# Performance work log

Measured on AMD Instinct MI355X. Metric: run time of the kernel, lower is better.

Reference implementation:

```python
import jax, jax.numpy as jnp
import numpy as np

SL, BS, D, H = 2048, 4, 512, 8
NH = D // H  # per-head dim (nhid)
SCALE = np.float32(1.0 / np.sqrt(NH))


def setup_inputs() -> dict:
    key = jax.random.key(0)
    ks = jax.random.split(key, 8)
    s = np.float32(0.02)
    return {
        "input_tensor": jax.random.normal(ks[0], (SL, BS, D), jnp.float32),
        "keys_vector": jax.random.normal(ks[1], (SL, BS, D), jnp.float32),
        "values_vector": jax.random.normal(ks[2], (SL, BS, D), jnp.float32),
        # learned projections: query/keys/values -> num_heads*nhid, plus output proj
        "Wq": jax.random.normal(ks[3], (D, D), jnp.float32) * s,
        "bq": jnp.zeros((D,), jnp.float32),
        "Wk": jax.random.normal(ks[4], (D, D), jnp.float32) * s,
        "bk": jnp.zeros((D,), jnp.float32),
        "Wv": jax.random.normal(ks[5], (D, D), jnp.float32) * s,
        "bv": jnp.zeros((D,), jnp.float32),
        "Wo": jax.random.normal(ks[6], (D, D), jnp.float32) * s,
        "bo": jnp.zeros((D,), jnp.float32),
    }


def reference(input_tensor, keys_vector, values_vector, Wq, bq, Wk, bk, Wv, bv, Wo, bo):
    # Vectorized equivalent of the per-step Python loop with incremental mask
    # (mask=True): query step i attends to keys 0..i -> causal attention.
    q = (input_tensor @ Wq + bq).reshape(SL, BS, H, NH)   # [q,b,h,n]
    k = (keys_vector @ Wk + bk).reshape(SL, BS, H, NH)    # [s,b,h,n]
    v = (values_vector @ Wv + bv).reshape(SL, BS, H, NH)  # [s,b,h,n]
    scores = jnp.einsum('qbhn,sbhn->qsbh', q, k) * SCALE  # [q,s,b,h]
    causal = jnp.tril(jnp.ones((SL, SL), dtype=bool))     # allow s <= q
    scores = jnp.where(causal[:, :, None, None], scores, jnp.float32(-1e9))
    w = jax.nn.softmax(scores, axis=1)                    # softmax over keys s
    out = jnp.einsum('qsbh,sbhn->qbhn', w, v).reshape(SL, BS, D)
    return out @ Wo + bo                                  # [q,b,D]
```

## Files before the change

kernel.cpp:

```cpp
#include <hip/hip_runtime.h>

typedef __attribute__((ext_vector_type(8))) short short8;
typedef __attribute__((ext_vector_type(4))) short short4v;
typedef __attribute__((ext_vector_type(4))) float f32x4;
typedef __attribute__((ext_vector_type(2))) unsigned int uint2v;

constexpr int SL = 2048, BS = 4, D = 512, H = 8, NH = 64;
constexpr int M_ROWS = SL * BS;
constexpr float SCALE = 0.125f;
constexpr float LOG2E = 1.44269504088896340736f;

__device__ __forceinline__ unsigned short f2bf(float f) {
  union { float f; unsigned u; } v; v.f = f;
  unsigned r = v.u + 0x7FFFu + ((v.u >> 16) & 1u);
  return (unsigned short)(r >> 16);
}

__device__ __forceinline__ unsigned cvt_pk_bf16(float a, float b) {
  unsigned r;
  asm("v_cvt_pk_bf16_f32 %0, %1, %2" : "=v"(r) : "v"(a), "v"(b));
  return r;
}

__device__ __forceinline__ float fast_exp2(float x) {
  float r;
  asm("v_exp_f32 %0, %1" : "=v"(r) : "v"(x));
  return r;
}

__device__ __forceinline__ void gl16(const void* g, void* l) {
  __builtin_amdgcn_global_load_lds(
      (const __attribute__((address_space(1))) unsigned int*)g,
      (__attribute__((address_space(3))) unsigned int*)l, 16, 0, 0);
}

__global__ __launch_bounds__(256) void prep_wt(
    const float* __restrict__ w0, const float* __restrict__ w1,
    const float* __restrict__ w2, const float* __restrict__ w3,
    unsigned short* __restrict__ wtb) {
  __shared__ float tl[64][65];
  const int tid = threadIdx.x;
  const int wi = blockIdx.x >> 6, t6 = blockIdx.x & 63;
  const int k0 = (t6 >> 3) * 64, n0 = (t6 & 7) * 64;
  const float* W = wi == 0 ? w0 : (wi == 1 ? w1 : (wi == 2 ? w2 : w3));
  unsigned short* WT = wtb + (size_t)wi * D * D;

#pragma unroll
  for (int i = 0; i < 4; ++i) {
    int k = (tid >> 4) + i * 16, n4 = (tid & 15) * 4;
    f32x4 v = *reinterpret_cast<const f32x4*>(&W[(size_t)(k0 + k) * D + n0 + n4]);
#pragma unroll
    for (int j = 0; j < 4; ++j) tl[n4 + j][k] = v[j];
  }
  __syncthreads();
#pragma unroll
  for (int i = 0; i < 2; ++i) {
    int n = (tid >> 3) + i * 32, k8 = (tid & 7) * 8;
    union { unsigned u[4]; short8 s; } pk;
#pragma unroll
    for (int j = 0; j < 4; ++j)
      pk.u[j] = cvt_pk_bf16(tl[n][k8 + 2 * j], tl[n][k8 + 2 * j + 1]);
    *reinterpret_cast<short8*>(&WT[(size_t)(n0 + n) * D + k0 + k8]) = pk.s;
  }
}

template <bool A_BF16, int OUT_MODE>
__device__ __forceinline__ void gemm_bt_body(const void* __restrict__ Ap,
                                             const unsigned short* __restrict__ BT,
                                             const float* __restrict__ bias,
                                             void* __restrict__ Outp, float scale,
                                             unsigned short* smem) {
  const int tid = threadIdx.x;
  const int brow = blockIdx.x * 128;
  const int bcol = blockIdx.y * 128;
  const int lane = tid & 63;
  const int wid = tid >> 6;
  const int wr = (wid >> 1) * 64;
  const int wc = (wid & 1) * 64;
  const int r = lane & 15;
  const int g = lane >> 4;

  auto a_buf = [&](int b) { return smem + b * 16384; };
  auto b_buf = [&](int b) { return smem + b * 16384 + 8192; };

  f32x4 acc[4][4];
#pragma unroll
  for (int m = 0; m < 4; ++m)
#pragma unroll
    for (int n = 0; n < 4; ++n) acc[m][n] = f32x4{0.f, 0.f, 0.f, 0.f};

  auto STAGE_B = [&](int kt, int bsel) {
    unsigned short* bl = b_buf(bsel);
#pragma unroll
    for (int j = 0; j < 4; ++j) {
      int c = j * 256 + tid;
      int row = c >> 3, c8 = (c & 7) ^ (row & 7);
      gl16(&BT[(size_t)(bcol + row) * D + kt + c8 * 8], &bl[c * 8]);
    }
  };
  auto STAGE_A_LDS = [&](int kt, int bsel) {
    const unsigned short* A = (const unsigned short*)Ap;
    unsigned short* al = a_buf(bsel);
#pragma unroll
    for (int j = 0; j < 4; ++j) {
      int c = j * 256 + tid;
      int row = c >> 3, c8 = (c & 7) ^ (row & 7);
      gl16(&A[(size_t)(brow + row) * D + kt + c8 * 8], &al[c * 8]);
    }
  };
  auto A_LOAD = [&](int kt, f32x4 (&va)[4][2]) {
    const float* A = (const float*)Ap;
#pragma unroll
    for (int j = 0; j < 4; ++j) {
      int c = j * 256 + tid;
      int row = c >> 3, c8 = (c & 7) ^ (row & 7);
      const float* ap = &A[(size_t)(brow + row) * D + kt + c8 * 8];
      va[j][0] = *reinterpret_cast<const f32x4*>(ap);
      va[j][1] = *reinterpret_cast<const f32x4*>(ap + 4);
    }
  };
  auto A_WRITE = [&](f32x4 (&va)[4][2], int bsel) {
    unsigned short* al = a_buf(bsel);
#pragma unroll
    for (int j = 0; j < 4; ++j) {
      int c = j * 256 + tid;
      union { unsigned u[4]; short8 s; } pk;
      pk.u[0] = cvt_pk_bf16(va[j][0][0], va[j][0][1]);
      pk.u[1] = cvt_pk_bf16(va[j][0][2], va[j][0][3]);
      pk.u[2] = cvt_pk_bf16(va[j][1][0], va[j][1][1]);
      pk.u[3] = cvt_pk_bf16(va[j][1][2], va[j][1][3]);
      *reinterpret_cast<short8*>(&al[c * 8]) = pk.s;
    }
  };
  auto COMPUTE = [&](int bsel) {
    const unsigned short* al = a_buf(bsel);
    const unsigned short* bl = b_buf(bsel);
#pragma unroll
    for (int kk2 = 0; kk2 < 2; ++kk2) {
      short8 af[4], bfr[4];
#pragma unroll
      for (int m = 0; m < 4; ++m)
        af[m] = *reinterpret_cast<const short8*>(
            &al[(wr + m * 16 + r) * 64 + (((kk2 * 4 + g) ^ (r & 7)) * 8)]);
#pragma unroll
      for (int n = 0; n < 4; ++n)
        bfr[n] = *reinterpret_cast<const short8*>(
            &bl[(wc + n * 16 + r) * 64 + (((kk2 * 4 + g) ^ (r & 7)) * 8)]);
      __builtin_amdgcn_s_setprio(1);
#pragma unroll
      for (int m = 0; m < 4; ++m)
#pragma unroll
        for (int n = 0; n < 4; ++n)
          acc[m][n] = __builtin_amdgcn_mfma_f32_16x16x32_bf16(af[m], bfr[n], acc[m][n], 0, 0, 0);
      __builtin_amdgcn_s_setprio(0);
    }
  };

  if (A_BF16) {
    STAGE_A_LDS(0, 0);
    STAGE_B(0, 0);
    asm volatile("s_waitcnt vmcnt(0)" ::: "memory");
  } else {
    f32x4 va[4][2];
    A_LOAD(0, va);
    STAGE_B(0, 0);
    asm volatile("s_waitcnt vmcnt(4)" ::: "memory");
    A_WRITE(va, 0);
    asm volatile("s_waitcnt vmcnt(0) lgkmcnt(0)" ::: "memory");
  }
  __builtin_amdgcn_s_barrier();

#pragma unroll
  for (int t = 0; t < 8; ++t) {
    const int cur = t & 1, nxt = cur ^ 1;
    const int ktn = (t + 1) * 64;
    __builtin_amdgcn_sched_barrier(0);
    f32x4 va[4][2];
    if (t < 7) {
      if (A_BF16) {
        STAGE_A_LDS(ktn, nxt);
        STAGE_B(ktn, nxt);
      } else {
        A_LOAD(ktn, va);
        STAGE_B(ktn, nxt);
      }
    }
    __builtin_amdgcn_sched_barrier(0);
    COMPUTE(cur);
    if (t < 7) {
      if (!A_BF16) {
        asm volatile("s_waitcnt vmcnt(4)" ::: "memory");
        A_WRITE(va, nxt);
      }
      asm volatile("s_waitcnt vmcnt(0) lgkmcnt(0)" ::: "memory");
      __builtin_amdgcn_s_barrier();
    }
  }

  if (OUT_MODE == 2) {
    unsigned short* sc = smem;
    const int wr4 = wr >> 2;
#pragma unroll
    for (int m = 0; m < 4; ++m)
#pragma unroll
      for (int n = 0; n < 4; ++n) {
        int col = wc + n * 16 + r;
        float bv = bias[bcol + col];
        int sl = wr4 + m * 4 + g;
#pragma unroll
        for (int rr = 0; rr < 4; ++rr) {
          int c = (rr * 4 + (sl >> 3)) ^ (col & 7);
          sc[col * 128 + c * 8 + (sl & 7)] = f2bf((acc[m][n][rr] + bv) * scale);
        }
      }
    asm volatile("s_waitcnt lgkmcnt(0)" ::: "memory");
    __builtin_amdgcn_s_barrier();
    unsigned short* VT = (unsigned short*)Outp;
#pragma unroll
    for (int i2 = 0; i2 < 2; ++i2) {
      int q = tid * 2 + i2;
      int col = q >> 2, bb = q & 3;
      int gcol = bcol + col, hh = gcol >> 6, nh = gcol & 63;
      size_t gbase = (((size_t)bb * H + hh) * NH + nh) * SL + (brow >> 2);
#pragma unroll
      for (int j = 0; j < 4; ++j) {
        short8 v = *reinterpret_cast<const short8*>(
            &sc[col * 128 + (((bb * 4 + j) ^ (col & 7)) * 8)]);
        *reinterpret_cast<short8*>(&VT[gbase + j * 8]) = v;
      }
    }
  } else {
#pragma unroll
    for (int m = 0; m < 4; ++m)
#pragma unroll
      for (int n = 0; n < 4; ++n) {
        int gcol = bcol + wc + n * 16 + r;
        float bv = bias[gcol];
#pragma unroll
        for (int rr = 0; rr < 4; ++rr) {
          int grow = brow + wr + m * 16 + g * 4 + rr;
          float val = (acc[m][n][rr] + bv) * scale;
          if (OUT_MODE == 0)
            ((float*)Outp)[(size_t)grow * D + gcol] = val;
          else
            ((unsigned short*)Outp)[(size_t)grow * D + gcol] = f2bf(val);
        }
      }
  }
}

__global__ __launch_bounds__(256, 2) void qkv_gemm(
    const float* __restrict__ x0, const float* __restrict__ x1, const float* __restrict__ x2,
    const unsigned short* __restrict__ wtb,
    const float* __restrict__ b0, const float* __restrict__ b1, const float* __restrict__ b2,
    unsigned short* __restrict__ q_out, unsigned short* __restrict__ k_out,
    unsigned short* __restrict__ vt_out) {
  __shared__ __align__(16) unsigned short smem[2 * 16384];
  int z = blockIdx.z;
  const float* X = z == 0 ? x0 : (z == 1 ? x1 : x2);
  const unsigned short* WT = wtb + (size_t)z * D * D;
  const float* B = z == 0 ? b0 : (z == 1 ? b1 : b2);
  float scale = (z == 0) ? SCALE * LOG2E : 1.0f;
  if (z == 2)
    gemm_bt_body<false, 2>(X, WT, B, vt_out, scale, smem);
  else
    gemm_bt_body<false, 1>(X, WT, B, z == 0 ? q_out : k_out, scale, smem);
}

__global__ __launch_bounds__(256, 2) void gemm_oproj(
    const unsigned short* __restrict__ A, const unsigned short* __restrict__ WT,
    const float* __restrict__ B, float* __restrict__ Outp) {
  __shared__ __align__(16) unsigned short smem[2 * 16384];
  gemm_bt_body<true, 0>(A, WT, B, Outp, 1.0f, smem);
}

__global__ __launch_bounds__(256, 4) void flash_attn(
    const unsigned short* __restrict__ Q, const unsigned short* __restrict__ K,
    const unsigned short* __restrict__ Vt, unsigned short* __restrict__ O) {
  __shared__ __align__(16) unsigned short k_lds[2][64 * 64];
  __shared__ __align__(16) unsigned short v_lds[2][64 * 64];
  __shared__ __align__(16) unsigned short p_lds[4][16 * 64];

  const int bid = blockIdx.x;
  const int s = bid >> 5, idx = bid & 31;
  const int grp = idx & 7;
  const int bh = grp * 4 + (idx >> 3);
  const int b = bh >> 3, h = bh & 7;
  const int qt = (s < 8) ? 31 - s : (s < 16) ? s + 8 : (s < 24) ? 31 - s : s - 24;
  const int q0 = qt * 64;

  const int tid = threadIdx.x;
  const int w = tid >> 6, lane = tid & 63;
  const int r = lane & 15, g = lane >> 4;
  const int swz = (r & 7) << 3;

  const unsigned short* Qb = Q + (size_t)b * D + h * NH;
  const unsigned short* Kb = K + (size_t)b * D + h * NH;
  const unsigned short* Vb = Vt + ((size_t)(b * H + h) * NH) * SL;
  unsigned short* Ob = O + (size_t)b * D + h * NH;
  unsigned short* pw = &p_lds[w][0];

  auto STAGE = [&](int kt, int bsel) {
    unsigned short* kl = &k_lds[bsel][0];
    unsigned short* vl = &v_lds[bsel][0];
#pragma unroll
    for (int j = 0; j < 2; ++j) {
      int c = j * 256 + tid;
      int row = c >> 3, c8 = (c & 7) ^ (row & 7);
      gl16(&Kb[(size_t)(kt * 64 + row) * (BS * D) + c8 * 8], &kl[c * 8]);
      gl16(&Vb[(size_t)row * SL + kt * 64 + c8 * 8], &vl[c * 8]);
    }
  };

  STAGE(0, 0);

  short8 qf[2];
#pragma unroll
  for (int kk = 0; kk < 2; ++kk)
    qf[kk] = *reinterpret_cast<const short8*>(
        &Qb[(size_t)(q0 + w * 16 + r) * (BS * D) + kk * 32 + g * 8]);

  f32x4 oa[4];
#pragma unroll
  for (int n = 0; n < 4; ++n) oa[n] = f32x4{0.f, 0.f, 0.f, 0.f};
  float mr = -1e30f, lrp = 0.f;

  for (int kt = 0; kt <= qt; ++kt) {
    asm volatile("s_waitcnt vmcnt(0)" ::: "memory");
    __builtin_amdgcn_s_barrier();
    __builtin_amdgcn_sched_barrier(0);
    if (kt + 1 <= qt) STAGE(kt + 1, (kt + 1) & 1);

    const int bsel = kt & 1;
    const unsigned short* kl = &k_lds[bsel][0];
    const unsigned short* vl = &v_lds[bsel][0];
    short8 kf[2][4], vt[2][4];
#pragma unroll
    for (int kk = 0; kk < 2; ++kk)
#pragma unroll
      for (int n = 0; n < 4; ++n)
        kf[kk][n] = *reinterpret_cast<const short8*>(
            &kl[(n * 16 + r) * 64 + (((kk * 4 + g) ^ (r & 7)) * 8)]);

    f32x4 sv[4];
#pragma unroll
    for (int n = 0; n < 4; ++n) sv[n] = f32x4{0.f, 0.f, 0.f, 0.f};
#pragma unroll
    for (int kk = 0; kk < 2; ++kk) {
      __builtin_amdgcn_s_setprio(1);
#pragma unroll
      for (int n = 0; n < 4; ++n)
        sv[n] = __builtin_amdgcn_mfma_f32_16x16x32_bf16(kf[kk][n], qf[kk], sv[n], 0, 0, 0);
      __builtin_amdgcn_s_setprio(0);
    }

#pragma unroll
    for (int kk = 0; kk < 2; ++kk)
#pragma unroll
      for (int n = 0; n < 4; ++n)
        vt[kk][n] = *reinterpret_cast<const short8*>(
            &vl[(n * 16 + r) * 64 + (((kk * 4 + g) ^ (r & 7)) * 8)]);

    if (kt == qt) {
      int qrow = q0 + w * 16 + r;
#pragma unroll
      for (int n = 0; n < 4; ++n)
#pragma unroll
        for (int rr = 0; rr < 4; ++rr)
          if (kt * 64 + n * 16 + g * 4 + rr > qrow) sv[n][rr] = -1e30f;
    }

    float t0 = fmaxf(fmaxf(sv[0][0], sv[0][1]), sv[0][2]);
    float t1 = fmaxf(fmaxf(sv[0][3], sv[1][0]), sv[1][1]);
    float t2 = fmaxf(fmaxf(sv[1][2], sv[1][3]), sv[2][0]);
    float t3 = fmaxf(fmaxf(sv[2][1], sv[2][2]), sv[2][3]);
    float t4 = fmaxf(fmaxf(sv[3][0], sv[3][1]), sv[3][2]);
    float mxl = fmaxf(fmaxf(fmaxf(t0, t1), fmaxf(t2, t3)), fmaxf(t4, sv[3][3]));
    bool need = __any(mxl > mr + 8.f);
    float mold = mr;
    float mnew = mold;
    if (need) {
      float mx = fmaxf(mxl, __shfl_xor(mxl, 16));
      mx = fmaxf(mx, __shfl_xor(mx, 32));
      mnew = fmaxf(mold, mx);
    }
#pragma unroll
    for (int n = 0; n < 4; ++n)
#pragma unroll
      for (int rr = 0; rr < 4; ++rr)
        sv[n][rr] = fast_exp2(sv[n][rr] - mnew);
    float a0 = (sv[0][0] + sv[0][1]) + (sv[0][2] + sv[0][3]);
    float a1 = (sv[1][0] + sv[1][1]) + (sv[1][2] + sv[1][3]);
    float a2 = (sv[2][0] + sv[2][1]) + (sv[2][2] + sv[2][3]);
    float a3 = (sv[3][0] + sv[3][1]) + (sv[3][2] + sv[3][3]);
    float psl = (a0 + a1) + (a2 + a3);
    if (need) {
      float sf = fast_exp2(mold - mnew);
      mr = mnew;
      lrp = lrp * sf + psl;
#pragma unroll
      for (int n = 0; n < 4; ++n) oa[n] *= sf;
    } else {
      lrp += psl;
    }

#pragma unroll
    for (int n = 0; n < 4; ++n) {
      uint2v pk;
      pk.x = cvt_pk_bf16(sv[n][0], sv[n][1]);
      pk.y = cvt_pk_bf16(sv[n][2], sv[n][3]);
      *reinterpret_cast<uint2v*>(&pw[r * 64 + ((n * 16 + g * 4) ^ swz)]) = pk;
    }
    asm volatile("s_waitcnt lgkmcnt(0)" ::: "memory");
    __builtin_amdgcn_sched_barrier(0);

    short8 pf[2];
#pragma unroll
    for (int kk = 0; kk < 2; ++kk)
      pf[kk] = *reinterpret_cast<const short8*>(
          &pw[r * 64 + (((kk * 4 + g) ^ (r & 7)) * 8)]);
#pragma unroll
    for (int kk = 0; kk < 2; ++kk) {
      __builtin_amdgcn_s_setprio(1);
#pragma unroll
      for (int n = 0; n < 4; ++n)
        oa[n] = __builtin_amdgcn_mfma_f32_16x16x32_bf16(vt[kk][n], pf[kk], oa[n], 0, 0, 0);
      __builtin_amdgcn_s_setprio(0);
    }
  }

  {
    float lr = lrp + __shfl_xor(lrp, 16);
    lr += __shfl_xor(lr, 32);
    float inv = 1.0f / lr;
#pragma unroll
    for (int n = 0; n < 4; ++n) {
      uint2v pk;
      pk.x = cvt_pk_bf16(oa[n][0] * inv, oa[n][1] * inv);
      pk.y = cvt_pk_bf16(oa[n][2] * inv, oa[n][3] * inv);
      *reinterpret_cast<uint2v*>(&pw[r * 64 + ((n * 16 + g * 4) ^ swz)]) = pk;
    }
    asm volatile("s_waitcnt lgkmcnt(0)" ::: "memory");
    __builtin_amdgcn_sched_barrier(0);
#pragma unroll
    for (int i2 = 0; i2 < 2; ++i2) {
      int c = i2 * 64 + lane;
      int row = c >> 3, c8 = c & 7;
      short8 v = *reinterpret_cast<const short8*>(&pw[row * 64 + c8 * 8]);
      *reinterpret_cast<short8*>(
          &Ob[(size_t)(q0 + w * 16 + row) * (BS * D) + ((c8 ^ (row & 7)) * 8)]) = v;
    }
  }
}

extern "C" void kernel_launch(void* const* d_in, const int* in_sizes, int n_in,
                              void* d_out, int out_size, void* d_ws, size_t ws_size,
                              hipStream_t stream) {
  const float* x  = (const float*)d_in[0];
  const float* kx = (const float*)d_in[1];
  const float* vx = (const float*)d_in[2];
  const float* Wq = (const float*)d_in[3];
  const float* bq = (const float*)d_in[4];
  const float* Wk = (const float*)d_in[5];
  const float* bk = (const float*)d_in[6];
  const float* Wv = (const float*)d_in[7];
  const float* bv = (const float*)d_in[8];
  const float* Wo = (const float*)d_in[9];
  const float* bo = (const float*)d_in[10];

  unsigned short* ws = (unsigned short*)d_ws;
  unsigned short* qb  = ws;
  unsigned short* kb  = ws + (size_t)M_ROWS * D;
  unsigned short* vtb = ws + (size_t)M_ROWS * D * 2;
  unsigned short* wtb = ws + (size_t)M_ROWS * D * 3;

  prep_wt<<<dim3(256), dim3(256), 0, stream>>>(Wq, Wk, Wv, Wo, wtb);
  qkv_gemm<<<dim3(64, 4, 3), dim3(256), 0, stream>>>(x, kx, vx, wtb, bq, bk, bv,
                                                     qb, kb, vtb);
  flash_attn<<<dim3(1024), dim3(256), 0, stream>>>(qb, kb, vtb, qb);
  gemm_oproj<<<dim3(64, 4, 1), dim3(256), 0, stream>>>(qb, wtb + (size_t)3 * D * D,
                                                       bo, (float*)d_out);
}
```

Baseline: 81.67 us.

## Keep softmax probabilities in registers by permuting V fragment layout

Drops the per-iteration round trip of P through LDS: probabilities are converted to bf16 and packed straight into MFMA B-operand registers. The V fragment reads are changed to two 4-element loads in a permuted k-order that matches the register layout of the S accumulator. This removes LDS writes, a waitcnt and a sched barrier from each iteration, and frees the p_lds buffer. The epilogue now reuses k_lds behind a __syncthreads, and the split V loads double the number of LDS read instructions.

```diff
diff --git a/kernel.cpp b/kernel.cpp
--- a/kernel.cpp
+++ b/kernel.cpp
@@ -279,7 +279,6 @@
     const unsigned short* __restrict__ Vt, unsigned short* __restrict__ O) {
   __shared__ __align__(16) unsigned short k_lds[2][64 * 64];
   __shared__ __align__(16) unsigned short v_lds[2][64 * 64];
-  __shared__ __align__(16) unsigned short p_lds[4][16 * 64];
 
   const int bid = blockIdx.x;
   const int s = bid >> 5, idx = bid & 31;
@@ -298,7 +297,6 @@
   const unsigned short* Kb = K + (size_t)b * D + h * NH;
   const unsigned short* Vb = Vt + ((size_t)(b * H + h) * NH) * SL;
   unsigned short* Ob = O + (size_t)b * D + h * NH;
-  unsigned short* pw = &p_lds[w][0];
 
   auto STAGE = [&](int kt, int bsel) {
     unsigned short* kl = &k_lds[bsel][0];
@@ -334,13 +332,13 @@
     const int bsel = kt & 1;
     const unsigned short* kl = &k_lds[bsel][0];
     const unsigned short* vl = &v_lds[bsel][0];
-    short8 kf[2][4], vt[2][4];
+    short8 kf[2][4];
 #pragma unroll
     for (int kk = 0; kk < 2; ++kk)
 #pragma unroll
       for (int n = 0; n < 4; ++n)
         kf[kk][n] = *reinterpret_cast<const short8*>(
-            &kl[(n * 16 + r) * 64 + (((kk * 4 + g) ^ (r & 7)) * 8)]);
+            &kl[(n * 16 + r) * 64 + ((kk * 32 + g * 8) ^ swz)]);
 
     f32x4 sv[4];
 #pragma unroll
@@ -354,12 +352,17 @@
       __builtin_amdgcn_s_setprio(0);
     }
 
+    short8 vt[2][4];
 #pragma unroll
     for (int kk = 0; kk < 2; ++kk)
 #pragma unroll
-      for (int n = 0; n < 4; ++n)
-        vt[kk][n] = *reinterpret_cast<const short8*>(
-            &vl[(n * 16 + r) * 64 + (((kk * 4 + g) ^ (r & 7)) * 8)]);
+      for (int n = 0; n < 4; ++n) {
+        int base = (kk * 32 + g * 4) ^ swz;
+        union { short4v h[2]; short8 s8; } u;
+        u.h[0] = *reinterpret_cast<const short4v*>(&vl[(n * 16 + r) * 64 + base]);
+        u.h[1] = *reinterpret_cast<const short4v*>(&vl[(n * 16 + r) * 64 + (base ^ 16)]);
+        vt[kk][n] = u.s8;
+      }
 
     if (kt == qt) {
       int qrow = q0 + w * 16 + r;
@@ -404,21 +407,17 @@
       lrp += psl;
     }
 
-#pragma unroll
-    for (int n = 0; n < 4; ++n) {
-      uint2v pk;
-      pk.x = cvt_pk_bf16(sv[n][0], sv[n][1]);
-      pk.y = cvt_pk_bf16(sv[n][2], sv[n][3]);
-      *reinterpret_cast<uint2v*>(&pw[r * 64 + ((n * 16 + g * 4) ^ swz)]) = pk;
-    }
-    asm volatile("s_waitcnt lgkmcnt(0)" ::: "memory");
-    __builtin_amdgcn_sched_barrier(0);
-
     short8 pf[2];
 #pragma unroll
-    for (int kk = 0; kk < 2; ++kk)
-      pf[kk] = *reinterpret_cast<const short8*>(
-          &pw[r * 64 + (((kk * 4 + g) ^ (r & 7)) * 8)]);
+    for (int kk = 0; kk < 2; ++kk) {
+      union { unsigned u[4]; short8 s8; } P;
+      P.u[0] = cvt_pk_bf16(sv[2 * kk][0], sv[2 * kk][1]);
+      P.u[1] = cvt_pk_bf16(sv[2 * kk][2], sv[2 * kk][3]);
+      P.u[2] = cvt_pk_bf16(sv[2 * kk + 1][0], sv[2 * kk + 1][1]);
+      P.u[3] = cvt_pk_bf16(sv[2 * kk + 1][2], sv[2 * kk + 1][3]);
+      pf[kk] = P.s8;
+    }
+
 #pragma unroll
     for (int kk = 0; kk < 2; ++kk) {
       __builtin_amdgcn_s_setprio(1);
@@ -429,7 +428,9 @@
     }
   }
 
+  __syncthreads();
   {
+    unsigned short* pw = &k_lds[0][0] + w * 2048;
     float lr = lrp + __shfl_xor(lrp, 16);
     lr += __shfl_xor(lr, 32);
     float inv = 1.0f / lr;
```

After: 82.80 us. No clear change (+1.4%).
